# Kernel tuning notes

Hardware: AMD Instinct MI355X
Metric: run time of the kernel (lower is better)

## Reference

```python
import jax, jax.numpy as jnp
import numpy as np

ALPHA = 0.2  # LeakyReLU negative slope


def setup_inputs() -> dict:
    key = jax.random.key(0)
    k1, k2, k3, k4 = jax.random.split(key, 4)
    B, N, F_in, F_out = 16, 2048, 64, 64
    h = jax.random.normal(k1, (B, N, F_in), dtype=jnp.float32)
    bias_mat = jnp.zeros((B, N, N), dtype=jnp.float32)
    # xavier_uniform with gain=1.414
    def xavier(k, shape, gain=1.414):
        fan_in, fan_out = shape[0], shape[1]
        bound = gain * np.sqrt(6.0 / (fan_in + fan_out))
        return jax.random.uniform(k, shape, jnp.float32, -bound, bound)
    W = xavier(k2, (F_in, F_out))
    a1 = xavier(k3, (F_out, 1))
    a2 = xavier(k4, (F_out, 1))
    return {"h": h, "bias_mat": bias_mat, "W": W, "a1": a1, "a2": a2}


def reference(h, bias_mat, W, a1, a2):
    # h: [B, N, F_in]; W: [F_in, F_out]
    Wh = jnp.einsum("bnf,fo->bno", h, W)            # [B, N, F_out]
    Wh1 = jnp.einsum("bno,oi->bni", Wh, a1)          # [B, N, 1]
    Wh2 = jnp.einsum("bno,oi->bni", Wh, a2)          # [B, N, 1]
    e = Wh1 + jnp.swapaxes(Wh2, 1, 2)                # [B, N, N] additive scores
    e = jax.nn.leaky_relu(e, negative_slope=ALPHA) + bias_mat
    attention = jax.nn.softmax(e, axis=2)            # row-wise over neighbors
    h_prime = jnp.einsum("bnm,bmo->bno", attention, Wh)
    return h_prime
```

## Files before the change

### kernel.cpp

```cpp
#include <hip/hip_runtime.h>
#include <hip/hip_bf16.h>
#include <cstdint>
#include <cstddef>

#define ALPHA 0.2f
#define LOG2E 1.4426950408889634f

using f32x4 = __attribute__((ext_vector_type(4))) float;
using s16x8 = __attribute__((ext_vector_type(8))) short;

typedef __attribute__((address_space(3))) unsigned lds_u32;
typedef __attribute__((address_space(1))) const unsigned glb_u32;

__device__ __forceinline__ unsigned f2bf(float f) {
  unsigned u = __float_as_uint(f);
  u = (u + 0x7fffu + ((u >> 16) & 1u)) >> 16;
  return u;
}

__global__ __launch_bounds__(256) void k1_proj(
    const float* __restrict__ h, const float* __restrict__ W,
    const float* __restrict__ a1, const float* __restrict__ a2,
    unsigned short* __restrict__ whT, float* __restrict__ s1,
    float* __restrict__ s2) {
  __shared__ __align__(16) float h_lds[64 * 64];
  __shared__ __align__(16) float W_lds[64 * 64];
  __shared__ __align__(16) unsigned short t_lds[64 * 64];

  const int t = threadIdx.x;
  const int c = t & 63;
  const int w = t >> 6;
  const int row0 = blockIdx.x * 64;

  const float4* hg = (const float4*)(h + (size_t)row0 * 64);
  #pragma unroll
  for (int r = 0; r < 4; ++r) {
    ((float4*)h_lds)[t + r * 256] = hg[t + r * 256];
    ((float4*)W_lds)[t + r * 256] = ((const float4*)W)[t + r * 256];
  }
  const float a1v = a1[c];
  const float a2v = a2[c];
  __syncthreads();

  float acc[16];
  #pragma unroll
  for (int r = 0; r < 16; ++r) acc[r] = 0.0f;

  #pragma unroll 1
  for (int kc = 0; kc < 16; ++kc) {
    const float w0 = W_lds[(kc * 4 + 0) * 64 + c];
    const float w1 = W_lds[(kc * 4 + 1) * 64 + c];
    const float w2 = W_lds[(kc * 4 + 2) * 64 + c];
    const float w3 = W_lds[(kc * 4 + 3) * 64 + c];
    #pragma unroll
    for (int r = 0; r < 16; ++r) {
      const float4 hv = *(const float4*)(h_lds + (w * 16 + r) * 64 + kc * 4);
      acc[r] = fmaf(hv.x, w0, acc[r]);
      acc[r] = fmaf(hv.y, w1, acc[r]);
      acc[r] = fmaf(hv.z, w2, acc[r]);
      acc[r] = fmaf(hv.w, w3, acc[r]);
    }
  }

  #pragma unroll 1
  for (int r = 0; r < 16; ++r) {
    float v1 = acc[r] * a1v;
    float v2 = acc[r] * a2v;
    #pragma unroll
    for (int s = 1; s < 64; s <<= 1) {
      v1 += __shfl_xor(v1, s, 64);
      v2 += __shfl_xor(v2, s, 64);
    }
    if (c == 0) {
      s1[row0 + w * 16 + r] = v1;
      s2[row0 + w * 16 + r] = v2;
    }
  }

  #pragma unroll
  for (int hh = 0; hh < 2; ++hh) {
    uint4 pk;
    pk.x = f2bf(acc[hh * 8 + 0]) | (f2bf(acc[hh * 8 + 1]) << 16);
    pk.y = f2bf(acc[hh * 8 + 2]) | (f2bf(acc[hh * 8 + 3]) << 16);
    pk.z = f2bf(acc[hh * 8 + 4]) | (f2bf(acc[hh * 8 + 5]) << 16);
    pk.w = f2bf(acc[hh * 8 + 6]) | (f2bf(acc[hh * 8 + 7]) << 16);
    const int off = c * 128 + ((w * 32 + hh * 16) ^ ((c & 7) << 4));
    *(uint4*)((char*)t_lds + off) = pk;
  }
  __syncthreads();

  const int b = row0 >> 11;
  const int n0 = row0 & 2047;
  #pragma unroll
  for (int q = 0; q < 2; ++q) {
    const int chunk = q * 256 + t;
    const int cc = chunk >> 3;
    const int w8 = (chunk & 7) * 16;
    const uint4 v =
        *(const uint4*)((const char*)t_lds + cc * 128 + (w8 ^ ((cc & 7) << 4)));
    *(uint4*)((char*)whT + ((size_t)(b * 64 + cc) * 2048 + n0) * 2 + w8) = v;
  }
}

__global__ __launch_bounds__(256, 2) void k2_attn(
    const float* __restrict__ bias, const unsigned short* __restrict__ whT,
    const float* __restrict__ s1g, const float* __restrict__ s2g,
    float* __restrict__ out) {
  __shared__ __align__(16) unsigned short wbuf[4][4096];
  __shared__ __align__(16) float s2_lds[2048];

  const int t = threadIdx.x;
  const int lane = t & 63;
  const int w = t >> 6;
  const int arow = lane & 15;
  const int kgrp = lane >> 4;
  const int b = blockIdx.x >> 5;
  const int i0 = (blockIdx.x & 31) * 64;
  const int gi = i0 + w * 16 + arow;

  const float s1v = s1g[b * 2048 + gi];

  #pragma unroll
  for (int q = 0; q < 2; ++q)
    ((float4*)s2_lds)[t + q * 256] =
        ((const float4*)(s2g + b * 2048))[t + q * 256];
  __syncthreads();

  const char* whT_b = (const char*)whT + (size_t)b * 64 * 2048 * 2;
  const float* bias_p = bias + ((size_t)b * 2048 + gi) * 2048 + kgrp * 8;

  const int src_swz = ((lane & 7) * 16) ^ ((lane >> 3) << 4);
  const char* gsrc0 = whT_b + (size_t)(lane >> 3) * 4096 + src_swz;

  auto whT_gll = [&](int jt) {
    char* dst = (char*)wbuf + (jt & 3) * 8192;
    #pragma unroll
    for (int q = 0; q < 2; ++q) {
      const int chunk = w * 2 + q;
      __builtin_amdgcn_global_load_lds(
          (glb_u32*)(gsrc0 + (size_t)chunk * 8 * 4096 + jt * 128),
          (lds_u32*)(dst + chunk * 1024), 16, 0, 0);
    }
  };
  auto bias_load = [&](f32x4 (&dst)[4], int jt) {
    const float* p = bias_p + jt * 64;
    dst[0] = *(const f32x4*)(p);
    dst[1] = *(const f32x4*)(p + 4);
    dst[2] = *(const f32x4*)(p + 32);
    dst[3] = *(const f32x4*)(p + 36);
  };

  f32x4 acc[4];
  #pragma unroll
  for (int ct = 0; ct < 4; ++ct) acc[ct] = (f32x4){0.f, 0.f, 0.f, 0.f};
  float m = -INFINITY, l = 0.0f;

  f32x4 biasA[4], biasB[4];
  bias_load(biasA, 0);
  whT_gll(0);
  whT_gll(1);
  bias_load(biasB, 1);

  auto body = [&](int jt, f32x4 (&bcur)[4]) {
    if (jt + 2 < 32) whT_gll(jt + 2);

    float ev[16];
    #pragma unroll
    for (int f = 0; f < 2; ++f) {
      const f32x4 sa = *(const f32x4*)(s2_lds + jt * 64 + f * 32 + kgrp * 8);
      const f32x4 sb =
          *(const f32x4*)(s2_lds + jt * 64 + f * 32 + kgrp * 8 + 4);
      const f32x4 ba = bcur[f * 2 + 0];
      const f32x4 bb = bcur[f * 2 + 1];
      #pragma unroll
      for (int e = 0; e < 4; ++e) {
        float x = s1v + sa[e];
        x = x > 0.0f ? x : ALPHA * x;
        ev[f * 8 + e] = x + ba[e];
        float y = s1v + sb[e];
        y = y > 0.0f ? y : ALPHA * y;
        ev[f * 8 + 4 + e] = y + bb[e];
      }
    }

    float mx = ev[0];
    #pragma unroll
    for (int e = 1; e < 16; ++e) mx = fmaxf(mx, ev[e]);
    mx = fmaxf(mx, __shfl_xor(mx, 16, 64));
    mx = fmaxf(mx, __shfl_xor(mx, 32, 64));
    const float mnew = fmaxf(m, mx);
    const float corr = exp2f((m - mnew) * LOG2E);

    float ps = 0.0f;
    s16x8 afrag[2];
    #pragma unroll
    for (int f = 0; f < 2; ++f) {
      #pragma unroll
      for (int e = 0; e < 8; ++e) {
        const float p = exp2f((ev[f * 8 + e] - mnew) * LOG2E);
        ps += p;
        afrag[f][e] = (short)f2bf(p);
      }
    }
    ps += __shfl_xor(ps, 16, 64);
    ps += __shfl_xor(ps, 32, 64);
    l = l * corr + ps;
    m = mnew;

    float fc[4];
    #pragma unroll
    for (int r = 0; r < 4; ++r) fc[r] = __shfl(corr, kgrp * 4 + r, 64);
    #pragma unroll
    for (int ct = 0; ct < 4; ++ct) {
      acc[ct][0] *= fc[0];
      acc[ct][1] *= fc[1];
      acc[ct][2] *= fc[2];
      acc[ct][3] *= fc[3];
    }

    if (jt + 2 < 32) bias_load(bcur, jt + 2);

    asm volatile("s_waitcnt vmcnt(12)" ::: "memory");
    asm volatile("s_barrier" ::: "memory");

    const char* mybuf = (const char*)wbuf + (jt & 3) * 8192;
    #pragma unroll
    for (int ct = 0; ct < 4; ++ct) {
      const int cc = ct * 16 + arow;
      #pragma unroll
      for (int f = 0; f < 2; ++f) {
        const s16x8 bfrag = *(const s16x8*)(
            mybuf + cc * 128 + ((f * 64 + kgrp * 16) ^ ((cc & 7) << 4)));
        asm("s_nop 1\n\t"
            "v_mfma_f32_16x16x32_bf16 %0, %1, %2, %0"
            : "+v"(acc[ct])
            : "v"(afrag[f]), "v"(bfrag));
      }
    }
  };

  #pragma unroll 1
  for (int jt = 0; jt < 32; jt += 2) {
    body(jt + 0, biasA);
    body(jt + 1, biasB);
  }

  asm volatile("s_nop 7\n\ts_nop 7" ::: "memory");

  const float linv = 1.0f / l;
  #pragma unroll
  for (int r = 0; r < 4; ++r) {
    const float li = __shfl(linv, kgrp * 4 + r, 64);
    float* op = out + ((size_t)b * 2048 + i0 + w * 16 + kgrp * 4 + r) * 64;
    #pragma unroll
    for (int ct = 0; ct < 4; ++ct) op[ct * 16 + arow] = acc[ct][r] * li;
  }
}

extern "C" void kernel_launch(void* const* d_in, const int* in_sizes, int n_in,
                              void* d_out, int out_size, void* d_ws,
                              size_t ws_size, hipStream_t stream) {
  const float* h = (const float*)d_in[0];
  const float* bias = (const float*)d_in[1];
  const float* W = (const float*)d_in[2];
  const float* a1 = (const float*)d_in[3];
  const float* a2 = (const float*)d_in[4];
  float* out = (float*)d_out;

  char* ws = (char*)d_ws;
  unsigned short* whT = (unsigned short*)ws;
  float* s1 = (float*)(ws + 4 * 1024 * 1024);
  float* s2 = (float*)(ws + 4 * 1024 * 1024 + 128 * 1024);

  k1_proj<<<dim3(512), dim3(256), 0, stream>>>(h, W, a1, a2, whT, s1, s2);
  k2_attn<<<dim3(512), dim3(256), 0, stream>>>(bias, whT, s1, s2, out);
}
```

Before: 83.07 us.

## Deepen bias prefetch to four-tile macro-blocks with explicit vmcnt scheduling

The per-tile bias prefetch (two tiles ahead, four f32x4 per tile) becomes a macro-block scheme. Sixteen f32x4 of bias covering four tiles are issued at once, one macro-block ahead, into double-buffered register arrays. Per-subtile s_waitcnt counts are hand-tuned so the whT LDS loads are waited on while bias loads stay in flight. The aim is to hide the latency of the large bias stream better, at the cost of more VGPRs (32 f32x4 of bias) and fragile hard-coded wait counts.

```diff
diff --git a/kernel.cpp b/kernel.cpp
--- a/kernel.cpp
+++ b/kernel.cpp
@@ -102,6 +102,8 @@
   }
 }
 
+#define FENCE asm volatile("" ::: "memory")
+
 __global__ __launch_bounds__(256, 2) void k2_attn(
     const float* __restrict__ bias, const unsigned short* __restrict__ whT,
     const float* __restrict__ s1g, const float* __restrict__ s2g,
@@ -127,7 +129,8 @@
   __syncthreads();
 
   const char* whT_b = (const char*)whT + (size_t)b * 64 * 2048 * 2;
-  const float* bias_p = bias + ((size_t)b * 2048 + gi) * 2048 + kgrp * 8;
+  const char* bias_pb =
+      (const char*)(bias + ((size_t)b * 2048 + gi) * 2048) + kgrp * 32;
 
   const int src_swz = ((lane & 7) * 16) ^ ((lane >> 3) << 4);
   const char* gsrc0 = whT_b + (size_t)(lane >> 3) * 4096 + src_swz;
@@ -142,108 +145,127 @@
           (lds_u32*)(dst + chunk * 1024), 16, 0, 0);
     }
   };
-  auto bias_load = [&](f32x4 (&dst)[4], int jt) {
-    const float* p = bias_p + jt * 64;
-    dst[0] = *(const f32x4*)(p);
-    dst[1] = *(const f32x4*)(p + 4);
-    dst[2] = *(const f32x4*)(p + 32);
-    dst[3] = *(const f32x4*)(p + 36);
-  };
 
   f32x4 acc[4];
   #pragma unroll
   for (int ct = 0; ct < 4; ++ct) acc[ct] = (f32x4){0.f, 0.f, 0.f, 0.f};
   float m = -INFINITY, l = 0.0f;
 
-  f32x4 biasA[4], biasB[4];
-  bias_load(biasA, 0);
+  f32x4 bA[16], bB[16];
+
+#define BIAS_ISSUE(DST, mm)                                          \
+  {                                                                  \
+    const char* p_ = bias_pb + (size_t)(mm) * 1024;                  \
+    _Pragma("unroll") for (int s_ = 0; s_ < 4; ++s_) {               \
+      DST[s_ * 4 + 0] = *(const f32x4*)(p_ + s_ * 256 + 0);          \
+      DST[s_ * 4 + 1] = *(const f32x4*)(p_ + s_ * 256 + 16);         \
+      DST[s_ * 4 + 2] = *(const f32x4*)(p_ + s_ * 256 + 128);        \
+      DST[s_ * 4 + 3] = *(const f32x4*)(p_ + s_ * 256 + 144);        \
+    }                                                                \
+  }
+
+#define SUB_BODY(JT, CUR, SI, DO_GLL, BIAS_STMT, VM_STMT)                  \
+  {                                                                        \
+    const int jt_ = (JT);                                                  \
+    if (DO_GLL) whT_gll(jt_ + 2);                                          \
+    FENCE;                                                                 \
+    BIAS_STMT;                                                             \
+    FENCE;                                                                 \
+    float ev[16];                                                          \
+    _Pragma("unroll") for (int f = 0; f < 2; ++f) {                        \
+      const f32x4 sa =                                                     \
+          *(const f32x4*)(s2_lds + jt_ * 64 + f * 32 + kgrp * 8);          \
+      const f32x4 sb =                                                     \
+          *(const f32x4*)(s2_lds + jt_ * 64 + f * 32 + kgrp * 8 + 4);      \
+      const f32x4 ba = CUR[(SI) * 4 + f * 2 + 0];                          \
+      const f32x4 bb = CUR[(SI) * 4 + f * 2 + 1];                          \
+      _Pragma("unroll") for (int e = 0; e < 4; ++e) {                      \
+        float x = s1v + sa[e];                                             \
+        x = x > 0.0f ? x : ALPHA * x;                                      \
+        ev[f * 8 + e] = x + ba[e];                                         \
+        float y = s1v + sb[e];                                             \
+        y = y > 0.0f ? y : ALPHA * y;                                      \
+        ev[f * 8 + 4 + e] = y + bb[e];                                     \
+      }                                                                    \
+    }                                                                      \
+    float mx = ev[0];                                                      \
+    _Pragma("unroll") for (int e = 1; e < 16; ++e) mx = fmaxf(mx, ev[e]);  \
+    mx = fmaxf(mx, __shfl_xor(mx, 16, 64));                                \
+    mx = fmaxf(mx, __shfl_xor(mx, 32, 64));                                \
+    const float mnew = fmaxf(m, mx);                                       \
+    const float corr = exp2f((m - mnew) * LOG2E);                          \
+    float ps = 0.0f;                                                       \
+    s16x8 afrag[2];                                                        \
+    _Pragma("unroll") for (int f = 0; f < 2; ++f) {                        \
+      _Pragma("unroll") for (int e = 0; e < 8; ++e) {                      \
+        const float p = exp2f((ev[f * 8 + e] - mnew) * LOG2E);             \
+        ps += p;                                                           \
+        afrag[f][e] = (short)f2bf(p);                                      \
+      }                                                                    \
+    }                                                                      \
+    ps += __shfl_xor(ps, 16, 64);                                          \
+    ps += __shfl_xor(ps, 32, 64);                                          \
+    l = l * corr + ps;                                                     \
+    m = mnew;                                                              \
+    float fc[4];                                                           \
+    _Pragma("unroll") for (int r = 0; r < 4; ++r) fc[r] =                  \
+        __shfl(corr, kgrp * 4 + r, 64);                                    \
+    _Pragma("unroll") for (int ct = 0; ct < 4; ++ct) {                     \
+      acc[ct][0] *= fc[0];                                                 \
+      acc[ct][1] *= fc[1];                                                 \
+      acc[ct][2] *= fc[2];                                                 \
+      acc[ct][3] *= fc[3];                                                 \
+    }                                                                      \
+    VM_STMT;                                                               \
+    asm volatile("s_barrier" ::: "memory");                                \
+    const char* mybuf_ = (const char*)wbuf + (jt_ & 3) * 8192;             \
+    _Pragma("unroll") for (int ct = 0; ct < 4; ++ct) {                     \
+      const int cc = ct * 16 + arow;                                       \
+      _Pragma("unroll") for (int f = 0; f < 2; ++f) {                      \
+        const s16x8 bfrag = *(const s16x8*)(                               \
+            mybuf_ + cc * 128 + ((f * 64 + kgrp * 16) ^ ((cc & 7) << 4))); \
+        asm("s_nop 1\n\t"                                                  \
+            "v_mfma_f32_16x16x32_bf16 %0, %1, %2, %0"                      \
+            : "+v"(acc[ct])                                                \
+            : "v"(afrag[f]), "v"(bfrag));                                  \
+      }                                                                    \
+    }                                                                      \
+  }
+
+#define MB_STD(MM, CUR, NXT)                                          \
+  SUB_BODY((MM) * 4 + 0, CUR, 0, true, BIAS_ISSUE(NXT, (MM) + 1),     \
+           asm volatile("s_waitcnt vmcnt(20)" ::: "memory"));         \
+  SUB_BODY((MM) * 4 + 1, CUR, 1, true, (void)0,                       \
+           asm volatile("s_waitcnt vmcnt(20)" ::: "memory"));         \
+  SUB_BODY((MM) * 4 + 2, CUR, 2, true, (void)0,                       \
+           asm volatile("s_waitcnt vmcnt(20)" ::: "memory"));         \
+  SUB_BODY((MM) * 4 + 3, CUR, 3, true, (void)0,                       \
+           asm volatile("s_waitcnt vmcnt(4)" ::: "memory"));
+
+#define MB_LAST(CUR)                                                  \
+  SUB_BODY(28, CUR, 0, true, (void)0,                                 \
+           asm volatile("s_waitcnt vmcnt(4)" ::: "memory"));          \
+  SUB_BODY(29, CUR, 1, true, (void)0,                                 \
+           asm volatile("s_waitcnt vmcnt(4)" ::: "memory"));          \
+  SUB_BODY(30, CUR, 2, false, (void)0,                                \
+           asm volatile("s_waitcnt vmcnt(2)" ::: "memory"));          \
+  SUB_BODY(31, CUR, 3, false, (void)0,                                \
+           asm volatile("s_waitcnt vmcnt(0)" ::: "memory"));
+
+  BIAS_ISSUE(bA, 0);
+  FENCE;
   whT_gll(0);
   whT_gll(1);
-  bias_load(biasB, 1);
-
-  auto body = [&](int jt, f32x4 (&bcur)[4]) {
-    if (jt + 2 < 32) whT_gll(jt + 2);
-
-    float ev[16];
-    #pragma unroll
-    for (int f = 0; f < 2; ++f) {
-      const f32x4 sa = *(const f32x4*)(s2_lds + jt * 64 + f * 32 + kgrp * 8);
-      const f32x4 sb =
-          *(const f32x4*)(s2_lds + jt * 64 + f * 32 + kgrp * 8 + 4);
-      const f32x4 ba = bcur[f * 2 + 0];
-      const f32x4 bb = bcur[f * 2 + 1];
-      #pragma unroll
-      for (int e = 0; e < 4; ++e) {
-        float x = s1v + sa[e];
-        x = x > 0.0f ? x : ALPHA * x;
-        ev[f * 8 + e] = x + ba[e];
-        float y = s1v + sb[e];
-        y = y > 0.0f ? y : ALPHA * y;
-        ev[f * 8 + 4 + e] = y + bb[e];
-      }
-    }
-
-    float mx = ev[0];
-    #pragma unroll
-    for (int e = 1; e < 16; ++e) mx = fmaxf(mx, ev[e]);
-    mx = fmaxf(mx, __shfl_xor(mx, 16, 64));
-    mx = fmaxf(mx, __shfl_xor(mx, 32, 64));
-    const float mnew = fmaxf(m, mx);
-    const float corr = exp2f((m - mnew) * LOG2E);
-
-    float ps = 0.0f;
-    s16x8 afrag[2];
-    #pragma unroll
-    for (int f = 0; f < 2; ++f) {
-      #pragma unroll
-      for (int e = 0; e < 8; ++e) {
-        const float p = exp2f((ev[f * 8 + e] - mnew) * LOG2E);
-        ps += p;
-        afrag[f][e] = (short)f2bf(p);
-      }
-    }
-    ps += __shfl_xor(ps, 16, 64);
-    ps += __shfl_xor(ps, 32, 64);
-    l = l * corr + ps;
-    m = mnew;
-
-    float fc[4];
-    #pragma unroll
-    for (int r = 0; r < 4; ++r) fc[r] = __shfl(corr, kgrp * 4 + r, 64);
-    #pragma unroll
-    for (int ct = 0; ct < 4; ++ct) {
-      acc[ct][0] *= fc[0];
-      acc[ct][1] *= fc[1];
-      acc[ct][2] *= fc[2];
-      acc[ct][3] *= fc[3];
-    }
-
-    if (jt + 2 < 32) bias_load(bcur, jt + 2);
-
-    asm volatile("s_waitcnt vmcnt(12)" ::: "memory");
-    asm volatile("s_barrier" ::: "memory");
-
-    const char* mybuf = (const char*)wbuf + (jt & 3) * 8192;
-    #pragma unroll
-    for (int ct = 0; ct < 4; ++ct) {
-      const int cc = ct * 16 + arow;
-      #pragma unroll
-      for (int f = 0; f < 2; ++f) {
-        const s16x8 bfrag = *(const s16x8*)(
-            mybuf + cc * 128 + ((f * 64 + kgrp * 16) ^ ((cc & 7) << 4)));
-        asm("s_nop 1\n\t"
-            "v_mfma_f32_16x16x32_bf16 %0, %1, %2, %0"
-            : "+v"(acc[ct])
-            : "v"(afrag[f]), "v"(bfrag));
-      }
-    }
-  };
+  FENCE;
 
   #pragma unroll 1
-  for (int jt = 0; jt < 32; jt += 2) {
-    body(jt + 0, biasA);
-    body(jt + 1, biasB);
-  }
+  for (int mp = 0; mp < 3; ++mp) {
+    const int m0 = mp * 2;
+    MB_STD(m0, bA, bB);
+    MB_STD(m0 + 1, bB, bA);
+  }
+  MB_STD(6, bA, bB);
+  MB_LAST(bB);
 
   asm volatile("s_nop 7\n\ts_nop 7" ::: "memory");
 
```

Result: slower. 94.44 us (+13.7%).
